# Kernel tuning notes

Hardware: AMD Instinct MI355X
Metric: run time of the kernel (lower is better)

Reference implementation:

```python
import jax, jax.numpy as jnp
import numpy as np

EMB_DIM = 1024
HEAD_SIZE = 64
B, T = 4, 4096


def setup_inputs() -> dict:
    key = jax.random.key(0)
    kx, kq, kk, kv = jax.random.split(key, 4)
    scale = 1.0 / np.sqrt(EMB_DIM)
    x = jax.random.normal(kx, (B, T, EMB_DIM), dtype=jnp.float32)
    # weights stored as [emb_dim, head_size] so projection is x @ W
    Wq = jax.random.normal(kq, (EMB_DIM, HEAD_SIZE), dtype=jnp.float32) * scale
    Wk = jax.random.normal(kk, (EMB_DIM, HEAD_SIZE), dtype=jnp.float32) * scale
    Wv = jax.random.normal(kv, (EMB_DIM, HEAD_SIZE), dtype=jnp.float32) * scale
    return {"x": x, "Wq": Wq, "Wk": Wk, "Wv": Wv}


def reference(x, Wq, Wk, Wv):
    # Single causal self-attention head. NOTE: original scales by emb_dim**-0.5
    # (d = x.shape[-1]), not head_size**-0.5 — we reproduce that faithfully.
    _, t, d = x.shape
    q = jnp.einsum('bte,eh->bth', x, Wq)
    k = jnp.einsum('bte,eh->bth', x, Wk)
    v = jnp.einsum('bte,eh->bth', x, Wv)
    wei = jnp.einsum('bth,bsh->bts', q, k) * (d ** -0.5)  # [B, T, T]
    causal = jnp.tril(jnp.ones((t, t), dtype=bool))
    wei = jnp.where(causal, wei, -jnp.inf)
    attn = jax.nn.softmax(wei, axis=-1)
    out = jnp.einsum('bts,bsh->bth', attn, v)  # [B, T, head_size]
    return out
```

## Files before the change

### kernel.cpp

```cpp
#include <hip/hip_runtime.h>
#include <hip/hip_bf16.h>

#define EMB   1024
#define HS    64
#define BATCH 4
#define SEQ   4096
#define MTOT  (BATCH*SEQ)

typedef float  f32x4 __attribute__((ext_vector_type(4)));
typedef short  s16x8 __attribute__((ext_vector_type(8)));
typedef __bf16 bf16x8 __attribute__((ext_vector_type(8)));

__device__ __forceinline__ unsigned short f2bf(float f) {
    unsigned int u = __float_as_uint(f);
    u = (u + 0x7fffu + ((u >> 16) & 1u)) >> 16;
    return (unsigned short)u;
}
__device__ __forceinline__ f32x4 mfma16(s16x8 a, s16x8 b, f32x4 c) {
    return __builtin_amdgcn_mfma_f32_16x16x32_bf16(
        __builtin_bit_cast(bf16x8, a), __builtin_bit_cast(bf16x8, b), c, 0, 0, 0);
}
__device__ __forceinline__ void ld_lds16(const unsigned short* g, unsigned short* l) {
    __builtin_amdgcn_global_load_lds(
        (const __attribute__((address_space(1))) unsigned int*)g,
        (__attribute__((address_space(3))) unsigned int*)l, 16, 0, 0);
}

__global__ __launch_bounds__(256) void pack_w(const float* __restrict__ Wq,
                                              const float* __restrict__ Wk,
                                              const float* __restrict__ Wv,
                                              unsigned short* __restrict__ wp) {
    int idx = blockIdx.x * 256 + threadIdx.x;
    int l = idx & 63;
    int s = (idx >> 6) & 31;
    int t = idx >> 11;
    const float* W = (t < 4) ? Wq : (t < 8) ? Wk : Wv;
    float scale = (t < 4) ? 0.03125f : 1.0f;
    int n  = ((t & 3) * 16) + (l & 15);
    int k0 = s * 32 + ((l >> 4) * 8);
    s16x8 v;
#pragma unroll
    for (int j = 0; j < 8; j++)
        v[j] = (short)f2bf(W[(size_t)(k0 + j) * HS + n] * scale);
    *(s16x8*)(wp + (size_t)idx * 8) = v;
}

__global__ __launch_bounds__(256) void proj(const float* __restrict__ x,
                                            const unsigned short* __restrict__ wp,
                                            unsigned short* __restrict__ qws,
                                            unsigned short* __restrict__ kws,
                                            unsigned short* __restrict__ vtws) {
    __shared__ unsigned short wpl[2][12 * 512];
    __shared__ unsigned short vt[64][72];
    int l = threadIdx.x & 63, w = threadIdx.x >> 6;
    int lane15 = l & 15, quad = l >> 4;
    int row0 = blockIdx.x * 64;

    auto stage = [&](int buf, int sg) {
#pragma unroll
        for (int j = 0; j < 3; j++) {
            int t = w + j * 4;
            ld_lds16(wp + ((size_t)(t * 32 + sg) * 64 + l) * 8,
                     &wpl[buf][t * 512]);
        }
    };

    const float* xr = x + (size_t)(row0 + w * 16 + lane15) * EMB + quad * 8;
    f32x4 acc[12] = {};

    stage(0, 0);
    float4 a0 = *(const float4*)(xr);
    float4 a1 = *(const float4*)(xr + 4);
    int buf = 0;
    for (int sg = 0; sg < 32; sg++) {
        __syncthreads();
        if (sg < 31) stage(buf ^ 1, sg + 1);
        float4 b0, b1;
        if (sg < 31) {
            b0 = *(const float4*)(xr + (sg + 1) * 32);
            b1 = *(const float4*)(xr + (sg + 1) * 32 + 4);
        }
        s16x8 af;
        af[0] = (short)f2bf(a0.x); af[1] = (short)f2bf(a0.y);
        af[2] = (short)f2bf(a0.z); af[3] = (short)f2bf(a0.w);
        af[4] = (short)f2bf(a1.x); af[5] = (short)f2bf(a1.y);
        af[6] = (short)f2bf(a1.z); af[7] = (short)f2bf(a1.w);
#pragma unroll
        for (int t = 0; t < 12; t++) {
            s16x8 bfr = *(const s16x8*)(&wpl[buf][t * 512 + l * 8]);
            acc[t] = mfma16(af, bfr, acc[t]);
        }
        a0 = b0; a1 = b1;
        buf ^= 1;
    }

#pragma unroll
    for (int r = 0; r < 4; r++) {
        int row = row0 + w * 16 + quad * 4 + r;
#pragma unroll
        for (int t = 0; t < 4; t++) {
            qws[(size_t)row * HS + t * 16 + lane15] = f2bf(acc[t][r]);
            kws[(size_t)row * HS + t * 16 + lane15] = f2bf(acc[t + 4][r]);
            vt[w * 16 + quad * 4 + r][t * 16 + lane15] = f2bf(acc[t + 8][r]);
        }
    }
    __syncthreads();
    int tt = threadIdx.x;
    int h = tt & 63, seg = tt >> 6;
    int b = row0 >> 12, tp0 = row0 & (SEQ - 1);
    unsigned short tmp[16];
#pragma unroll
    for (int j = 0; j < 16; j++) tmp[j] = vt[seg * 16 + j][h];
    unsigned short* dst = vtws + ((size_t)b * HS + h) * SEQ + tp0 + seg * 16;
    *(s16x8*)dst       = *(s16x8*)tmp;
    *(s16x8*)(dst + 8) = *(s16x8*)(tmp + 8);
}

__global__ __launch_bounds__(256) void attn_part(const unsigned short* __restrict__ qws,
                                                 const unsigned short* __restrict__ kws,
                                                 const unsigned short* __restrict__ vtws,
                                                 float* __restrict__ op,
                                                 float* __restrict__ lp) {
    __shared__ unsigned short ldsK[2][4096];
    __shared__ unsigned short ldsV[2][4096];
    __shared__ unsigned short plds[4][16][72];

    int l = threadIdx.x & 63;
    int w = threadIdx.x >> 6;
    int lane15 = l & 15, quad = l >> 4;

    int W = blockIdx.x;
    int b = W / 288;
    int g = W - b * 288;
    int n = 1;
    while (g >= 4 * n * (n + 1)) n++;
    int off = g - 4 * n * (n - 1);
    int oQ  = (unsigned)off / (unsigned)n;
    int Q   = 8 * (n - 1) + oQ;
    int c   = off - oQ * n;
    int lenT = Q + 1;
    int t0 = c * 8;
    int t1 = min(t0 + 8, lenT);
    int q0 = Q * 64 + w * 16;
    int diag = lenT - 1;

    auto stage = [&](int buf, int c0) {
#pragma unroll
        for (int j = 0; j < 2; j++) {
            int s = w + j * 4;
            int t = s >> 1, h = s & 1;
            ld_lds16(kws + ((size_t)b * SEQ + c0 + t * 16 + lane15) * HS
                         + h * 32 + quad * 8,
                     &ldsK[buf][s * 512]);
            ld_lds16(vtws + ((size_t)b * HS + t * 16 + lane15) * SEQ
                          + c0 + h * 32 + quad * 8,
                     &ldsV[buf][s * 512]);
        }
    };

    const unsigned short* qbase =
        qws + ((size_t)b * SEQ + q0 + lane15) * HS + quad * 8;
    s16x8 qf0 = *(const s16x8*)(qbase);
    s16x8 qf1 = *(const s16x8*)(qbase + 32);

    f32x4 o[4] = {};
    float lsum[4] = {0.f, 0.f, 0.f, 0.f};

    stage(0, t0 * 64);
    int buf = 0;
    for (int kt = t0; kt < t1; kt++) {
        __syncthreads();
        if (kt + 1 < t1) stage(buf ^ 1, (kt + 1) * 64);

        f32x4 sacc[4] = {};
#pragma unroll
        for (int t = 0; t < 4; t++) {
            s16x8 kf0 = *(const s16x8*)(&ldsK[buf][(2 * t) * 512 + l * 8]);
            s16x8 kf1 = *(const s16x8*)(&ldsK[buf][(2 * t + 1) * 512 + l * 8]);
            sacc[t] = mfma16(qf0, kf0, sacc[t]);
            sacc[t] = mfma16(qf1, kf1, sacc[t]);
        }

        if (kt == diag) {
            int c0 = kt * 64;
#pragma unroll
            for (int t = 0; t < 4; t++)
#pragma unroll
                for (int r = 0; r < 4; r++) {
                    int qrow = q0 + quad * 4 + r;
                    int kcol = c0 + t * 16 + lane15;
                    if (kcol > qrow) sacc[t][r] = -1e30f;
                }
        }

#pragma unroll
        for (int t = 0; t < 4; t++)
#pragma unroll
            for (int r = 0; r < 4; r++) {
                float p = __expf(sacc[t][r]);
                lsum[r] += p;
                plds[w][quad * 4 + r][t * 16 + lane15] = f2bf(p);
            }
        __builtin_amdgcn_s_waitcnt(0xC07F);

#pragma unroll
        for (int c2 = 0; c2 < 2; c2++) {
            s16x8 pf = *(const s16x8*)(&plds[w][lane15][c2 * 32 + quad * 8]);
#pragma unroll
            for (int t = 0; t < 4; t++) {
                s16x8 vf = *(const s16x8*)(&ldsV[buf][(2 * t + c2) * 512 + l * 8]);
                o[t] = mfma16(pf, vf, o[t]);
            }
        }
        buf ^= 1;
    }

#pragma unroll
    for (int r = 0; r < 4; r++) {
#pragma unroll
        for (int d = 1; d < 16; d <<= 1)
            lsum[r] += __shfl_xor(lsum[r], d, 64);
    }

    size_t slot = (size_t)b * 288 + g;
    float* ob = op + slot * 4096;
#pragma unroll
    for (int t = 0; t < 4; t++)
#pragma unroll
        for (int r = 0; r < 4; r++)
            ob[(w * 16 + quad * 4 + r) * 64 + t * 16 + lane15] = o[t][r];
    if (lane15 == 0) {
#pragma unroll
        for (int r = 0; r < 4; r++)
            lp[slot * 64 + w * 16 + quad * 4 + r] = lsum[r];
    }
}

__global__ __launch_bounds__(256) void attn_combine(const float* __restrict__ op,
                                                    const float* __restrict__ lp,
                                                    float* __restrict__ out) {
    int e = blockIdx.x * 256 + threadIdx.x;
    int c4 = (e & 15) * 4;
    int row = e >> 4;
    int b   = row >> 12;
    int tr  = row & (SEQ - 1);
    int Q   = tr >> 6;
    int r64 = tr & 63;
    int n   = (Q >> 3) + 1;
    int g0  = 4 * n * (n - 1) + (Q - 8 * (n - 1)) * n;
    f32x4 os = {0.f, 0.f, 0.f, 0.f};
    float ls = 0.f;
    for (int c = 0; c < n; c++) {
        size_t slot = (size_t)b * 288 + g0 + c;
        os += *(const f32x4*)(op + slot * 4096 + r64 * 64 + c4);
        ls += lp[slot * 64 + r64];
    }
    f32x4 r = os / ls;
    *(f32x4*)(out + (size_t)row * HS + c4) = r;
}

extern "C" void kernel_launch(void* const* d_in, const int* in_sizes, int n_in,
                              void* d_out, int out_size, void* d_ws, size_t ws_size,
                              hipStream_t stream) {
    const float* x  = (const float*)d_in[0];
    const float* Wq = (const float*)d_in[1];
    const float* Wk = (const float*)d_in[2];
    const float* Wv = (const float*)d_in[3];
    float* out = (float*)d_out;

    unsigned short* ws   = (unsigned short*)d_ws;
    unsigned short* wp   = ws;
    unsigned short* qws  = ws + 262144;
    unsigned short* kws  = ws + 1310720;
    unsigned short* vtws = ws + 2359296;
    float* op = (float*)(ws + 3407872);
    float* lp = op + 4718592;

    hipLaunchKernelGGL(pack_w,      dim3(96),   dim3(256), 0, stream, Wq, Wk, Wv, wp);
    hipLaunchKernelGGL(proj,        dim3(256),  dim3(256), 0, stream, x, wp, qws, kws, vtws);
    hipLaunchKernelGGL(attn_part,   dim3(1152), dim3(256), 0, stream, qws, kws, vtws, op, lp);
    hipLaunchKernelGGL(attn_combine,dim3(1024), dim3(256), 0, stream, op, lp, out);
}
```

Baseline: 165.7 us.

## Split projection over K into four partial blocks with separate combine kernel

The QKV projection is rewritten as split-K. Each of 512 blocks keeps its slice of the packed weights in registers and loops over 128-row strips, writing bf16 partial sums to a new workspace buffer. A new proj_combine kernel sums the four partials, writes Q and K, and transposes V. The goal is more blocks than the 256 available to the old 256-CU projection and no per-iteration LDS staging or barriers. The cost is an extra launch, extra global traffic for the partials, and precision loss from rounding partials to bf16 before summing. A packed bf16 conversion intrinsic is also used for the x conversion.

```diff
diff --git a/kernel.cpp b/kernel.cpp
--- a/kernel.cpp
+++ b/kernel.cpp
@@ -10,11 +10,26 @@
 typedef float  f32x4 __attribute__((ext_vector_type(4)));
 typedef short  s16x8 __attribute__((ext_vector_type(8)));
 typedef __bf16 bf16x8 __attribute__((ext_vector_type(8)));
+typedef __bf16 bf16x2 __attribute__((ext_vector_type(2)));
 
 __device__ __forceinline__ unsigned short f2bf(float f) {
     unsigned int u = __float_as_uint(f);
     u = (u + 0x7fffu + ((u >> 16) & 1u)) >> 16;
     return (unsigned short)u;
+}
+__device__ __forceinline__ unsigned int pkbf(float lo, float hi) {
+#if __has_builtin(__builtin_amdgcn_cvt_pk_bf16_f32)
+    return __builtin_bit_cast(unsigned int,
+        __builtin_amdgcn_cvt_pk_bf16_f32(lo, hi));
+#else
+    return (unsigned int)f2bf(lo) | ((unsigned int)f2bf(hi) << 16);
+#endif
+}
+__device__ __forceinline__ s16x8 cvt8(float4 a, float4 b) {
+    union { unsigned int u[4]; s16x8 v; } r;
+    r.u[0] = pkbf(a.x, a.y); r.u[1] = pkbf(a.z, a.w);
+    r.u[2] = pkbf(b.x, b.y); r.u[3] = pkbf(b.z, b.w);
+    return r.v;
 }
 __device__ __forceinline__ f32x4 mfma16(s16x8 a, s16x8 b, f32x4 c) {
     return __builtin_amdgcn_mfma_f32_16x16x32_bf16(
@@ -47,66 +62,88 @@
 
 __global__ __launch_bounds__(256) void proj(const float* __restrict__ x,
                                             const unsigned short* __restrict__ wp,
-                                            unsigned short* __restrict__ qws,
-                                            unsigned short* __restrict__ kws,
-                                            unsigned short* __restrict__ vtws) {
-    __shared__ unsigned short wpl[2][12 * 512];
-    __shared__ unsigned short vt[64][72];
+                                            unsigned short* __restrict__ pb) {
     int l = threadIdx.x & 63, w = threadIdx.x >> 6;
     int lane15 = l & 15, quad = l >> 4;
+    int strip = blockIdx.x >> 2;
+    int ks    = blockIdx.x & 3;
+
+    s16x8 bw[3][8];
+#pragma unroll
+    for (int j = 0; j < 3; j++)
+#pragma unroll
+        for (int s = 0; s < 8; s++)
+            bw[j][s] = *(const s16x8*)(
+                wp + ((size_t)((3 * w + j) * 32 + ks * 8 + s) * 64 + l) * 8);
+
+    for (int rg = 0; rg < 8; rg++) {
+        int row0 = strip * 128 + rg * 16;
+        const float* xp = x + (size_t)(row0 + lane15) * EMB + ks * 256 + quad * 8;
+        float4 xv[16];
+#pragma unroll
+        for (int s = 0; s < 8; s++) {
+            xv[2 * s]     = *(const float4*)(xp + s * 32);
+            xv[2 * s + 1] = *(const float4*)(xp + s * 32 + 4);
+        }
+        f32x4 acc[3] = {};
+#pragma unroll
+        for (int s = 0; s < 8; s++) {
+            s16x8 af = cvt8(xv[2 * s], xv[2 * s + 1]);
+#pragma unroll
+            for (int j = 0; j < 3; j++)
+                acc[j] = mfma16(af, bw[j][s], acc[j]);
+        }
+#pragma unroll
+        for (int r = 0; r < 4; r++) {
+            int row = row0 + quad * 4 + r;
+#pragma unroll
+            for (int j = 0; j < 3; j++)
+                pb[((size_t)ks * MTOT + row) * 192 + (3 * w + j) * 16 + lane15] =
+                    f2bf(acc[j][r]);
+        }
+    }
+}
+
+__global__ __launch_bounds__(256) void proj_combine(const unsigned short* __restrict__ pb,
+                                                    unsigned short* __restrict__ qws,
+                                                    unsigned short* __restrict__ kws,
+                                                    unsigned short* __restrict__ vtws) {
+    __shared__ unsigned short vt[64][72];
+    int tid = threadIdx.x;
     int row0 = blockIdx.x * 64;
 
-    auto stage = [&](int buf, int sg) {
-#pragma unroll
-        for (int j = 0; j < 3; j++) {
-            int t = w + j * 4;
-            ld_lds16(wp + ((size_t)(t * 32 + sg) * 64 + l) * 8,
-                     &wpl[buf][t * 512]);
-        }
-    };
-
-    const float* xr = x + (size_t)(row0 + w * 16 + lane15) * EMB + quad * 8;
-    f32x4 acc[12] = {};
-
-    stage(0, 0);
-    float4 a0 = *(const float4*)(xr);
-    float4 a1 = *(const float4*)(xr + 4);
-    int buf = 0;
-    for (int sg = 0; sg < 32; sg++) {
-        __syncthreads();
-        if (sg < 31) stage(buf ^ 1, sg + 1);
-        float4 b0, b1;
-        if (sg < 31) {
-            b0 = *(const float4*)(xr + (sg + 1) * 32);
-            b1 = *(const float4*)(xr + (sg + 1) * 32 + 4);
-        }
-        s16x8 af;
-        af[0] = (short)f2bf(a0.x); af[1] = (short)f2bf(a0.y);
-        af[2] = (short)f2bf(a0.z); af[3] = (short)f2bf(a0.w);
-        af[4] = (short)f2bf(a1.x); af[5] = (short)f2bf(a1.y);
-        af[6] = (short)f2bf(a1.z); af[7] = (short)f2bf(a1.w);
-#pragma unroll
-        for (int t = 0; t < 12; t++) {
-            s16x8 bfr = *(const s16x8*)(&wpl[buf][t * 512 + l * 8]);
-            acc[t] = mfma16(af, bfr, acc[t]);
-        }
-        a0 = b0; a1 = b1;
-        buf ^= 1;
-    }
-
-#pragma unroll
-    for (int r = 0; r < 4; r++) {
-        int row = row0 + w * 16 + quad * 4 + r;
-#pragma unroll
-        for (int t = 0; t < 4; t++) {
-            qws[(size_t)row * HS + t * 16 + lane15] = f2bf(acc[t][r]);
-            kws[(size_t)row * HS + t * 16 + lane15] = f2bf(acc[t + 4][r]);
-            vt[w * 16 + quad * 4 + r][t * 16 + lane15] = f2bf(acc[t + 8][r]);
-        }
+#pragma unroll
+    for (int k = 0; k < 6; k++) {
+        int c = tid + k * 256;
+        int off = c * 8;
+        int row = (unsigned)off / 192u;
+        int col = off - row * 192;
+        size_t base = ((size_t)row0 + row) * 192 + col;
+        union { s16x8 v; unsigned int u[4]; } p[4];
+#pragma unroll
+        for (int ksq = 0; ksq < 4; ksq++)
+            p[ksq].v = *(const s16x8*)(pb + (size_t)ksq * MTOT * 192 + base);
+        union { unsigned int u[4]; s16x8 v; } o;
+#pragma unroll
+        for (int i = 0; i < 4; i++) {
+            float lo = 0.f, hi = 0.f;
+#pragma unroll
+            for (int ksq = 0; ksq < 4; ksq++) {
+                unsigned int u = p[ksq].u[i];
+                lo += __uint_as_float(u << 16);
+                hi += __uint_as_float(u & 0xFFFF0000u);
+            }
+            o.u[i] = pkbf(lo, hi);
+        }
+        if (col < 64)
+            *(s16x8*)(qws + ((size_t)row0 + row) * HS + col) = o.v;
+        else if (col < 128)
+            *(s16x8*)(kws + ((size_t)row0 + row) * HS + col - 64) = o.v;
+        else
+            *(s16x8*)(&vt[row][col - 128]) = o.v;
     }
     __syncthreads();
-    int tt = threadIdx.x;
-    int h = tt & 63, seg = tt >> 6;
+    int h = tid & 63, seg = tid >> 6;
     int b = row0 >> 12, tp0 = row0 & (SEQ - 1);
     unsigned short tmp[16];
 #pragma unroll
@@ -273,11 +310,13 @@
     unsigned short* qws  = ws + 262144;
     unsigned short* kws  = ws + 1310720;
     unsigned short* vtws = ws + 2359296;
-    float* op = (float*)(ws + 3407872);
+    unsigned short* pb   = ws + 3407872;
+    float* op = (float*)(ws + 15990784);
     float* lp = op + 4718592;
 
     hipLaunchKernelGGL(pack_w,      dim3(96),   dim3(256), 0, stream, Wq, Wk, Wv, wp);
-    hipLaunchKernelGGL(proj,        dim3(256),  dim3(256), 0, stream, x, wp, qws, kws, vtws);
+    hipLaunchKernelGGL(proj,        dim3(512),  dim3(256), 0, stream, x, wp, pb);
+    hipLaunchKernelGGL(proj_combine,dim3(256),  dim3(256), 0, stream, pb, qws, kws, vtws);
     hipLaunchKernelGGL(attn_part,   dim3(1152), dim3(256), 0, stream, qws, kws, vtws, op, lp);
     hipLaunchKernelGGL(attn_combine,dim3(1024), dim3(256), 0, stream, op, lp, out);
 }
```

Measured after the change: 190.7 us. +15.1%, slower.

## Restructure projection: 16-row blocks, per-wave output tiles, register-prefetched weights

Applied to the files above, without the earlier changes.

The projection kernel now gives each block 16 rows instead of 64, so the grid grows from 256 to 1024 blocks. Each wave computes one 16-column slice of Q, K and V rather than all twelve tiles. Weight fragments are loaded straight from global memory into registers with a two-stage prefetch, replacing the LDS double buffer and its per-iteration barriers. fp32-to-bf16 conversion uses a packed conversion builtin where the compiler offers it. This should raise occupancy and parallelism across the GPU, but every wave now reads the same x rows four times and weights are re-fetched per block, which adds memory traffic.

```diff
diff --git a/kernel.cpp b/kernel.cpp
--- a/kernel.cpp
+++ b/kernel.cpp
@@ -15,6 +15,20 @@
     unsigned int u = __float_as_uint(f);
     u = (u + 0x7fffu + ((u >> 16) & 1u)) >> 16;
     return (unsigned short)u;
+}
+__device__ __forceinline__ unsigned int pkbf(float lo, float hi) {
+#if __has_builtin(__builtin_amdgcn_cvt_pk_bf16_f32)
+    return __builtin_bit_cast(unsigned int,
+        __builtin_amdgcn_cvt_pk_bf16_f32(lo, hi));
+#else
+    return (unsigned int)f2bf(lo) | ((unsigned int)f2bf(hi) << 16);
+#endif
+}
+__device__ __forceinline__ s16x8 cvt8(float4 a, float4 b) {
+    union { unsigned int u[4]; s16x8 v; } r;
+    r.u[0] = pkbf(a.x, a.y); r.u[1] = pkbf(a.z, a.w);
+    r.u[2] = pkbf(b.x, b.y); r.u[3] = pkbf(b.z, b.w);
+    return r.v;
 }
 __device__ __forceinline__ f32x4 mfma16(s16x8 a, s16x8 b, f32x4 c) {
     return __builtin_amdgcn_mfma_f32_16x16x32_bf16(
@@ -50,70 +64,61 @@
                                             unsigned short* __restrict__ qws,
                                             unsigned short* __restrict__ kws,
                                             unsigned short* __restrict__ vtws) {
-    __shared__ unsigned short wpl[2][12 * 512];
-    __shared__ unsigned short vt[64][72];
+    __shared__ unsigned short vt[16][72];
     int l = threadIdx.x & 63, w = threadIdx.x >> 6;
     int lane15 = l & 15, quad = l >> 4;
-    int row0 = blockIdx.x * 64;
-
-    auto stage = [&](int buf, int sg) {
-#pragma unroll
-        for (int j = 0; j < 3; j++) {
-            int t = w + j * 4;
-            ld_lds16(wp + ((size_t)(t * 32 + sg) * 64 + l) * 8,
-                     &wpl[buf][t * 512]);
-        }
-    };
-
-    const float* xr = x + (size_t)(row0 + w * 16 + lane15) * EMB + quad * 8;
-    f32x4 acc[12] = {};
-
-    stage(0, 0);
-    float4 a0 = *(const float4*)(xr);
-    float4 a1 = *(const float4*)(xr + 4);
-    int buf = 0;
-    for (int sg = 0; sg < 32; sg++) {
-        __syncthreads();
-        if (sg < 31) stage(buf ^ 1, sg + 1);
-        float4 b0, b1;
-        if (sg < 31) {
-            b0 = *(const float4*)(xr + (sg + 1) * 32);
-            b1 = *(const float4*)(xr + (sg + 1) * 32 + 4);
-        }
-        s16x8 af;
-        af[0] = (short)f2bf(a0.x); af[1] = (short)f2bf(a0.y);
-        af[2] = (short)f2bf(a0.z); af[3] = (short)f2bf(a0.w);
-        af[4] = (short)f2bf(a1.x); af[5] = (short)f2bf(a1.y);
-        af[6] = (short)f2bf(a1.z); af[7] = (short)f2bf(a1.w);
-#pragma unroll
-        for (int t = 0; t < 12; t++) {
-            s16x8 bfr = *(const s16x8*)(&wpl[buf][t * 512 + l * 8]);
-            acc[t] = mfma16(af, bfr, acc[t]);
-        }
-        a0 = b0; a1 = b1;
-        buf ^= 1;
+    int row0 = blockIdx.x * 16;
+
+    const float* xp = x + (size_t)(row0 + lane15) * EMB + quad * 8;
+    const unsigned short* wb0 = wp + (size_t)l * 8;
+
+    s16x8 wb[2][3];
+    float4 xb[2][2];
+#pragma unroll
+    for (int p = 0; p < 2; p++) {
+#pragma unroll
+        for (int j = 0; j < 3; j++)
+            wb[p][j] = *(const s16x8*)(wb0 + (size_t)((w + 4 * j) * 32 + p) * 512);
+        xb[p][0] = *(const float4*)(xp + p * 32);
+        xb[p][1] = *(const float4*)(xp + p * 32 + 4);
+    }
+
+    f32x4 acc[3] = {};
+#pragma unroll 2
+    for (int s = 0; s < 32; s++) {
+        int cur = s & 1;
+        s16x8 af = cvt8(xb[cur][0], xb[cur][1]);
+#pragma unroll
+        for (int j = 0; j < 3; j++)
+            acc[j] = mfma16(af, wb[cur][j], acc[j]);
+        if (s < 30) {
+#pragma unroll
+            for (int j = 0; j < 3; j++)
+                wb[cur][j] = *(const s16x8*)(
+                    wb0 + (size_t)((w + 4 * j) * 32 + s + 2) * 512);
+            xb[cur][0] = *(const float4*)(xp + (s + 2) * 32);
+            xb[cur][1] = *(const float4*)(xp + (s + 2) * 32 + 4);
+        }
     }
 
 #pragma unroll
     for (int r = 0; r < 4; r++) {
-        int row = row0 + w * 16 + quad * 4 + r;
-#pragma unroll
-        for (int t = 0; t < 4; t++) {
-            qws[(size_t)row * HS + t * 16 + lane15] = f2bf(acc[t][r]);
-            kws[(size_t)row * HS + t * 16 + lane15] = f2bf(acc[t + 4][r]);
-            vt[w * 16 + quad * 4 + r][t * 16 + lane15] = f2bf(acc[t + 8][r]);
-        }
+        int row = row0 + quad * 4 + r;
+        qws[(size_t)row * HS + w * 16 + lane15] = f2bf(acc[0][r]);
+        kws[(size_t)row * HS + w * 16 + lane15] = f2bf(acc[1][r]);
+        vt[quad * 4 + r][w * 16 + lane15] = f2bf(acc[2][r]);
     }
     __syncthreads();
-    int tt = threadIdx.x;
-    int h = tt & 63, seg = tt >> 6;
-    int b = row0 >> 12, tp0 = row0 & (SEQ - 1);
-    unsigned short tmp[16];
-#pragma unroll
-    for (int j = 0; j < 16; j++) tmp[j] = vt[seg * 16 + j][h];
-    unsigned short* dst = vtws + ((size_t)b * HS + h) * SEQ + tp0 + seg * 16;
-    *(s16x8*)dst       = *(s16x8*)tmp;
-    *(s16x8*)(dst + 8) = *(s16x8*)(tmp + 8);
+    if (threadIdx.x < 64) {
+        int h = threadIdx.x;
+        int b = row0 >> 12, tp0 = row0 & (SEQ - 1);
+        unsigned short tmp[16];
+#pragma unroll
+        for (int j = 0; j < 16; j++) tmp[j] = vt[j][h];
+        unsigned short* dst = vtws + ((size_t)b * HS + h) * SEQ + tp0;
+        *(s16x8*)dst       = *(s16x8*)tmp;
+        *(s16x8*)(dst + 8) = *(s16x8*)(tmp + 8);
+    }
 }
 
 __global__ __launch_bounds__(256) void attn_part(const unsigned short* __restrict__ qws,
@@ -277,7 +282,7 @@
     float* lp = op + 4718592;
 
     hipLaunchKernelGGL(pack_w,      dim3(96),   dim3(256), 0, stream, Wq, Wk, Wv, wp);
-    hipLaunchKernelGGL(proj,        dim3(256),  dim3(256), 0, stream, x, wp, qws, kws, vtws);
+    hipLaunchKernelGGL(proj,        dim3(1024), dim3(256), 0, stream, x, wp, qws, kws, vtws);
     hipLaunchKernelGGL(attn_part,   dim3(1152), dim3(256), 0, stream, qws, kws, vtws, op, lp);
     hipLaunchKernelGGL(attn_combine,dim3(1024), dim3(256), 0, stream, op, lp, out);
 }
```

New measurement: 171.3 us. 1.03x slower.
